# Optimization experiments

Measured on AMD Instinct MI355X. Metric: run time of the kernel, lower is better.

Reference implementation:

```python
import jax, jax.numpy as jnp
import numpy as np

N = 8192
IN_F = 64
OUT_F = 64
ALPHA = 0.2
NEG_INF = -9e15
DENSITY = 0.02


def _signed_sparse(key, shape, density):
    k1, k2 = jax.random.split(key)
    mask = jax.random.uniform(k1, shape) < density
    vals = jax.random.normal(k2, shape, dtype=jnp.float32)
    return jnp.where(mask, vals, 0.0)


def setup_inputs() -> dict:
    key = jax.random.key(0)
    k_h, k_na, k_ea, k_w, k_a = jax.random.split(key, 5)
    h = jax.random.normal(k_h, (N, IN_F), dtype=jnp.float32)
    node_adj = _signed_sparse(k_na, (N, N), DENSITY)
    edge_adj = _signed_sparse(k_ea, (N, N), DENSITY)
    # xavier_uniform with gain=1.414
    lim_w = 1.414 * np.sqrt(6.0 / (IN_F + OUT_F))
    W_att = jax.random.uniform(k_w, (IN_F, OUT_F), minval=-lim_w, maxval=lim_w, dtype=jnp.float32)
    lim_a = 1.414 * np.sqrt(6.0 / (OUT_F + 1))
    a = jax.random.uniform(k_a, (OUT_F, 1), minval=-lim_a, maxval=lim_a, dtype=jnp.float32)
    return {"h": h, "node_adj": node_adj, "edge_adj": edge_adj, "W_att": W_att, "a": a}


def reference(h, node_adj, edge_adj, W_att, a):
    # h: [N, F_in], node_adj/edge_adj: [N, N]
    h_att = h @ W_att                                   # [N, F_out]
    h_plus = (node_adj > 0).astype(h.dtype) @ h_att     # [N, F_out]
    h_minus = (node_adj < 0).astype(h.dtype) @ h_att    # [N, F_out]
    a_input = jnp.abs(h_plus - h_minus)                 # [N, F_out]
    e = jax.nn.leaky_relu(a_input @ a, ALPHA)           # [N, 1]
    e_row = e[:, 0][None, :]                            # broadcast: row i of scores = e^T
    scores = jnp.where(edge_adj != 0, e_row, jnp.float32(NEG_INF))  # [N, N]
    attention = jax.nn.softmax(scores, axis=1)          # [N, N]
    # dropout omitted (eval-mode reference)
    h_prime = (attention * edge_adj) @ h                # [N, F_in]
    return h_prime, attention
```

## Files before the change

kernel.cpp:

```cpp
#include <hip/hip_runtime.h>
#include <math.h>

#define NN 8192
#define FF 64
#define ALPHA 0.2f
#define ECAP 512
#define WCAP 256

typedef float vf4 __attribute__((ext_vector_type(4)));

__global__ __launch_bounds__(256) void k_hatt(const float* __restrict__ h,
                                              const float* __restrict__ W,
                                              float* __restrict__ h_att) {
    __shared__ float Ws[64 * 64];
    int t = threadIdx.x;
    for (int k = t; k < 64 * 64; k += 256) Ws[k] = W[k];
    __syncthreads();
    int idx = blockIdx.x * 256 + t;
    int r = idx >> 6, c = idx & 63;
    const float* hr = h + (size_t)r * FF;
    float acc = 0.f;
#pragma unroll
    for (int k = 0; k < 64; ++k) acc += hr[k] * Ws[k * 64 + c];
    h_att[idx] = acc;
}

__global__ __launch_bounds__(256) void k_e(const float* __restrict__ node_adj,
                                           const float* __restrict__ h_att,
                                           const float* __restrict__ a,
                                           float* __restrict__ e) {
    __shared__ int lists[4][ECAP];
    int t = threadIdx.x, w = t >> 6, lane = t & 63;
    int row = blockIdx.x * 4 + w;
    unsigned long long lmask = (1ull << lane) - 1ull;
    const vf4* rp = (const vf4*)(node_adj + (size_t)row * NN);
    int cnt = 0;
#pragma unroll 4
    for (int it = 0; it < 32; ++it) {
        int idx = it * 64 + lane;
        vf4 v = __builtin_nontemporal_load(rp + idx);
        int j0 = idx * 4;
        { bool nz = v.x != 0.f; unsigned long long m = __ballot(nz);
          if (nz) lists[w][cnt + __popcll(m & lmask)] = (v.x > 0.f) ? (j0 + 1) : -(j0 + 1);
          cnt += __popcll(m); }
        { bool nz = v.y != 0.f; unsigned long long m = __ballot(nz);
          if (nz) lists[w][cnt + __popcll(m & lmask)] = (v.y > 0.f) ? (j0 + 2) : -(j0 + 2);
          cnt += __popcll(m); }
        { bool nz = v.z != 0.f; unsigned long long m = __ballot(nz);
          if (nz) lists[w][cnt + __popcll(m & lmask)] = (v.z > 0.f) ? (j0 + 3) : -(j0 + 3);
          cnt += __popcll(m); }
        { bool nz = v.w != 0.f; unsigned long long m = __ballot(nz);
          if (nz) lists[w][cnt + __popcll(m & lmask)] = (v.w > 0.f) ? (j0 + 4) : -(j0 + 4);
          cnt += __popcll(m); }
    }
    __syncthreads();

    float acc = 0.f;
    for (int k = 0; k < cnt; ++k) {
        int code = lists[w][k];
        int j = (code < 0 ? -code : code) - 1;
        float hv = h_att[(size_t)j * FF + lane];
        acc += (code < 0) ? -hv : hv;
    }
    float v = fabsf(acc) * a[lane];
#pragma unroll
    for (int off = 32; off; off >>= 1) v += __shfl_down(v, off, 64);
    if (lane == 0) e[row] = (v > 0.f) ? v : ALPHA * v;
}

__global__ __launch_bounds__(256) void k_prep(const float* __restrict__ e,
                                              float* __restrict__ E) {
    __shared__ float red[256];
    int t = threadIdx.x;
    float lm = -3.0e38f;
    for (int k = t; k < NN; k += 256) lm = fmaxf(lm, e[k]);
    red[t] = lm; __syncthreads();
    for (int s = 128; s; s >>= 1) { if (t < s) red[t] = fmaxf(red[t], red[t + s]); __syncthreads(); }
    float m = red[0];
    int i = blockIdx.x * 256 + t;
    E[i] = __expf(e[i] - m);
}

__global__ __launch_bounds__(256) void k_att(const float* __restrict__ edge_adj,
                                             const float* __restrict__ E,
                                             const float* __restrict__ h,
                                             float* __restrict__ att_out,
                                             float* __restrict__ hprime) {
    __shared__ int   jseg[4][WCAP];
    __shared__ float vseg[4][WCAP];
    __shared__ float red[256];
    __shared__ float r4z[4];
    __shared__ int   cnts[4];
    int t = threadIdx.x, w = t >> 6, lane = t & 63;
    int row = blockIdx.x;
    unsigned long long lmask = (1ull << lane) - 1ull;

    const vf4* rp = (const vf4*)(edge_adj + (size_t)row * NN);
    const vf4* Ep = (const vf4*)E;
    vf4 o[8];
    float zloc = 0.f;
    int cnt = 0;
#pragma unroll
    for (int it = 0; it < 8; ++it) {
        int idx = it * 256 + t;
        vf4 v  = __builtin_nontemporal_load(rp + idx);
        vf4 Ev = Ep[idx];
        int j0 = idx * 4;
        { bool nz = v.x != 0.f; unsigned long long m = __ballot(nz);
          float ox = nz ? Ev.x : 0.f;
          if (nz) { int p = cnt + __popcll(m & lmask); jseg[w][p] = j0;     vseg[w][p] = v.x * Ev.x; }
          cnt += __popcll(m); zloc += ox; o[it].x = ox; }
        { bool nz = v.y != 0.f; unsigned long long m = __ballot(nz);
          float oy = nz ? Ev.y : 0.f;
          if (nz) { int p = cnt + __popcll(m & lmask); jseg[w][p] = j0 + 1; vseg[w][p] = v.y * Ev.y; }
          cnt += __popcll(m); zloc += oy; o[it].y = oy; }
        { bool nz = v.z != 0.f; unsigned long long m = __ballot(nz);
          float oz = nz ? Ev.z : 0.f;
          if (nz) { int p = cnt + __popcll(m & lmask); jseg[w][p] = j0 + 2; vseg[w][p] = v.z * Ev.z; }
          cnt += __popcll(m); zloc += oz; o[it].z = oz; }
        { bool nz = v.w != 0.f; unsigned long long m = __ballot(nz);
          float ow = nz ? Ev.w : 0.f;
          if (nz) { int p = cnt + __popcll(m & lmask); jseg[w][p] = j0 + 3; vseg[w][p] = v.w * Ev.w; }
          cnt += __popcll(m); zloc += ow; o[it].w = ow; }
    }
    if (lane == 0) cnts[w] = cnt;
#pragma unroll
    for (int off = 32; off; off >>= 1) zloc += __shfl_down(zloc, off, 64);
    if (lane == 0) r4z[w] = zloc;
    __syncthreads();
    float Z = r4z[0] + r4z[1] + r4z[2] + r4z[3];
    int tot = cnts[0] + cnts[1] + cnts[2] + cnts[3];
    float invZ = (tot > 0) ? 1.f / Z : 0.f;

    float acc = 0.f;
    for (int k = 0; k < cnt; ++k)
        acc += vseg[w][k] * h[(size_t)jseg[w][k] * FF + lane];
    red[t] = acc;
    __syncthreads();
    if (t < 64)
        hprime[(size_t)row * FF + t] = (red[t] + red[t + 64] + red[t + 128] + red[t + 192]) * invZ;

    vf4* ap = (vf4*)(att_out + (size_t)row * NN);
    float unif = 1.0f / NN;
#pragma unroll
    for (int it = 0; it < 8; ++it) {
        int idx = it * 256 + t;
        vf4 ov = o[it];
        ov.x *= invZ; ov.y *= invZ; ov.z *= invZ; ov.w *= invZ;
        if (tot == 0) { ov.x = unif; ov.y = unif; ov.z = unif; ov.w = unif; }
        __builtin_nontemporal_store(ov, ap + idx);
    }
}

extern "C" void kernel_launch(void* const* d_in, const int* in_sizes, int n_in,
                              void* d_out, int out_size, void* d_ws, size_t ws_size,
                              hipStream_t stream) {
    const float* h        = (const float*)d_in[0];
    const float* node_adj = (const float*)d_in[1];
    const float* edge_adj = (const float*)d_in[2];
    const float* W_att    = (const float*)d_in[3];
    const float* a        = (const float*)d_in[4];

    float* out    = (float*)d_out;
    float* hprime = out;
    float* att    = out + (size_t)NN * FF;

    float* h_att = (float*)d_ws;
    float* e_vec = h_att + (size_t)NN * FF;
    float* E_vec = e_vec + NN;

    k_hatt<<<(NN * FF) / 256, 256, 0, stream>>>(h, W_att, h_att);
    k_e<<<NN / 4, 256, 0, stream>>>(node_adj, h_att, a, e_vec);
    k_prep<<<NN / 256, 256, 0, stream>>>(e_vec, E_vec);
    k_att<<<NN, 256, 0, stream>>>(edge_adj, E_vec, h, att, hprime);
}
```

Before: 627.5 us.

## Process four sparse neighbors per wave with float4 gathers and mbcnt prefix

The sparse gather loops in the score and attention kernels are restructured so each wave handles four list entries per iteration: 16 lanes per entry each load a float4 of the 64-wide feature row. Partial sums are then combined with xor shuffles. Lane prefix counts now use the mbcnt intrinsics, and index/value pairs are packed into a single int2 shared entry. The lists are padded with zero entries so the loop can run in steps of four. This cuts serial loop iterations and widens memory accesses, in exchange for extra shuffle reductions and padding reads of row 0.

```diff
diff --git a/kernel.cpp b/kernel.cpp
--- a/kernel.cpp
+++ b/kernel.cpp
@@ -8,6 +8,11 @@
 #define WCAP 256
 
 typedef float vf4 __attribute__((ext_vector_type(4)));
+
+__device__ __forceinline__ unsigned mbcnt64(unsigned long long m) {
+    return __builtin_amdgcn_mbcnt_hi((unsigned)(m >> 32),
+           __builtin_amdgcn_mbcnt_lo((unsigned)m, 0u));
+}
 
 __global__ __launch_bounds__(256) void k_hatt(const float* __restrict__ h,
                                               const float* __restrict__ W,
@@ -32,7 +37,6 @@
     __shared__ int lists[4][ECAP];
     int t = threadIdx.x, w = t >> 6, lane = t & 63;
     int row = blockIdx.x * 4 + w;
-    unsigned long long lmask = (1ull << lane) - 1ull;
     const vf4* rp = (const vf4*)(node_adj + (size_t)row * NN);
     int cnt = 0;
 #pragma unroll 4
@@ -41,30 +45,45 @@
         vf4 v = __builtin_nontemporal_load(rp + idx);
         int j0 = idx * 4;
         { bool nz = v.x != 0.f; unsigned long long m = __ballot(nz);
-          if (nz) lists[w][cnt + __popcll(m & lmask)] = (v.x > 0.f) ? (j0 + 1) : -(j0 + 1);
+          if (nz) lists[w][cnt + mbcnt64(m)] = (v.x > 0.f) ? (j0 + 1) : -(j0 + 1);
           cnt += __popcll(m); }
         { bool nz = v.y != 0.f; unsigned long long m = __ballot(nz);
-          if (nz) lists[w][cnt + __popcll(m & lmask)] = (v.y > 0.f) ? (j0 + 2) : -(j0 + 2);
+          if (nz) lists[w][cnt + mbcnt64(m)] = (v.y > 0.f) ? (j0 + 2) : -(j0 + 2);
           cnt += __popcll(m); }
         { bool nz = v.z != 0.f; unsigned long long m = __ballot(nz);
-          if (nz) lists[w][cnt + __popcll(m & lmask)] = (v.z > 0.f) ? (j0 + 3) : -(j0 + 3);
+          if (nz) lists[w][cnt + mbcnt64(m)] = (v.z > 0.f) ? (j0 + 3) : -(j0 + 3);
           cnt += __popcll(m); }
         { bool nz = v.w != 0.f; unsigned long long m = __ballot(nz);
-          if (nz) lists[w][cnt + __popcll(m & lmask)] = (v.w > 0.f) ? (j0 + 4) : -(j0 + 4);
-          cnt += __popcll(m); }
-    }
-    __syncthreads();
-
-    float acc = 0.f;
-    for (int k = 0; k < cnt; ++k) {
-        int code = lists[w][k];
-        int j = (code < 0 ? -code : code) - 1;
-        float hv = h_att[(size_t)j * FF + lane];
-        acc += (code < 0) ? -hv : hv;
-    }
-    float v = fabsf(acc) * a[lane];
-#pragma unroll
-    for (int off = 32; off; off >>= 1) v += __shfl_down(v, off, 64);
+          if (nz) lists[w][cnt + mbcnt64(m)] = (v.w > 0.f) ? (j0 + 4) : -(j0 + 4);
+          cnt += __popcll(m); }
+    }
+    if (lane < 4) lists[w][cnt + lane] = 0;
+
+    int g = lane >> 4, fl = lane & 15;
+    const vf4* Hp = (const vf4*)h_att;
+    vf4 acc = {0.f, 0.f, 0.f, 0.f};
+    int cnt4 = (cnt + 3) & ~3;
+#pragma unroll 2
+    for (int k = 0; k < cnt4; k += 4) {
+        int code = lists[w][k + g];
+        float s = (code < 0) ? -1.f : (code > 0 ? 1.f : 0.f);
+        int aj = (code < 0) ? -code : code;
+        int j = (aj > 0) ? aj - 1 : 0;
+        vf4 hv = Hp[(size_t)j * 16 + fl];
+        acc.x += s * hv.x; acc.y += s * hv.y; acc.z += s * hv.z; acc.w += s * hv.w;
+    }
+    acc.x += __shfl_xor(acc.x, 16, 64); acc.y += __shfl_xor(acc.y, 16, 64);
+    acc.z += __shfl_xor(acc.z, 16, 64); acc.w += __shfl_xor(acc.w, 16, 64);
+    acc.x += __shfl_xor(acc.x, 32, 64); acc.y += __shfl_xor(acc.y, 32, 64);
+    acc.z += __shfl_xor(acc.z, 32, 64); acc.w += __shfl_xor(acc.w, 32, 64);
+
+    vf4 av = ((const vf4*)a)[fl];
+    float v = fabsf(acc.x) * av.x + fabsf(acc.y) * av.y +
+              fabsf(acc.z) * av.z + fabsf(acc.w) * av.w;
+    v += __shfl_down(v, 8, 64);
+    v += __shfl_down(v, 4, 64);
+    v += __shfl_down(v, 2, 64);
+    v += __shfl_down(v, 1, 64);
     if (lane == 0) e[row] = (v > 0.f) ? v : ALPHA * v;
 }
 
@@ -86,14 +105,12 @@
                                              const float* __restrict__ h,
                                              float* __restrict__ att_out,
                                              float* __restrict__ hprime) {
-    __shared__ int   jseg[4][WCAP];
-    __shared__ float vseg[4][WCAP];
-    __shared__ float red[256];
+    __shared__ int2 seg[4][WCAP];
+    __shared__ vf4  red4[64];
     __shared__ float r4z[4];
     __shared__ int   cnts[4];
     int t = threadIdx.x, w = t >> 6, lane = t & 63;
     int row = blockIdx.x;
-    unsigned long long lmask = (1ull << lane) - 1ull;
 
     const vf4* rp = (const vf4*)(edge_adj + (size_t)row * NN);
     const vf4* Ep = (const vf4*)E;
@@ -108,35 +125,49 @@
         int j0 = idx * 4;
         { bool nz = v.x != 0.f; unsigned long long m = __ballot(nz);
           float ox = nz ? Ev.x : 0.f;
-          if (nz) { int p = cnt + __popcll(m & lmask); jseg[w][p] = j0;     vseg[w][p] = v.x * Ev.x; }
+          if (nz) seg[w][cnt + mbcnt64(m)] = make_int2(j0,     __float_as_int(v.x * Ev.x));
           cnt += __popcll(m); zloc += ox; o[it].x = ox; }
         { bool nz = v.y != 0.f; unsigned long long m = __ballot(nz);
           float oy = nz ? Ev.y : 0.f;
-          if (nz) { int p = cnt + __popcll(m & lmask); jseg[w][p] = j0 + 1; vseg[w][p] = v.y * Ev.y; }
+          if (nz) seg[w][cnt + mbcnt64(m)] = make_int2(j0 + 1, __float_as_int(v.y * Ev.y));
           cnt += __popcll(m); zloc += oy; o[it].y = oy; }
         { bool nz = v.z != 0.f; unsigned long long m = __ballot(nz);
           float oz = nz ? Ev.z : 0.f;
-          if (nz) { int p = cnt + __popcll(m & lmask); jseg[w][p] = j0 + 2; vseg[w][p] = v.z * Ev.z; }
+          if (nz) seg[w][cnt + mbcnt64(m)] = make_int2(j0 + 2, __float_as_int(v.z * Ev.z));
           cnt += __popcll(m); zloc += oz; o[it].z = oz; }
         { bool nz = v.w != 0.f; unsigned long long m = __ballot(nz);
           float ow = nz ? Ev.w : 0.f;
-          if (nz) { int p = cnt + __popcll(m & lmask); jseg[w][p] = j0 + 3; vseg[w][p] = v.w * Ev.w; }
+          if (nz) seg[w][cnt + mbcnt64(m)] = make_int2(j0 + 3, __float_as_int(v.w * Ev.w));
           cnt += __popcll(m); zloc += ow; o[it].w = ow; }
     }
     if (lane == 0) cnts[w] = cnt;
 #pragma unroll
     for (int off = 32; off; off >>= 1) zloc += __shfl_down(zloc, off, 64);
     if (lane == 0) r4z[w] = zloc;
+    if (lane < 4) seg[w][cnt + lane] = make_int2(0, 0);
     __syncthreads();
     float Z = r4z[0] + r4z[1] + r4z[2] + r4z[3];
     int tot = cnts[0] + cnts[1] + cnts[2] + cnts[3];
     float invZ = (tot > 0) ? 1.f / Z : 0.f;
 
-    float acc = 0.f;
-    for (int k = 0; k < cnt; ++k)
-        acc += vseg[w][k] * h[(size_t)jseg[w][k] * FF + lane];
-    red[t] = acc;
+    int g = lane >> 4, fl = lane & 15;
+    const vf4* Hp = (const vf4*)h;
+    vf4 acc = {0.f, 0.f, 0.f, 0.f};
+    int cnt4 = (cnt + 3) & ~3;
+#pragma unroll 2
+    for (int k = 0; k < cnt4; k += 4) {
+        int2 sv = seg[w][k + g];
+        float vv = __int_as_float(sv.y);
+        vf4 hv = Hp[(size_t)sv.x * 16 + fl];
+        acc.x += vv * hv.x; acc.y += vv * hv.y; acc.z += vv * hv.z; acc.w += vv * hv.w;
+    }
+    acc.x += __shfl_xor(acc.x, 16, 64); acc.y += __shfl_xor(acc.y, 16, 64);
+    acc.z += __shfl_xor(acc.z, 16, 64); acc.w += __shfl_xor(acc.w, 16, 64);
+    acc.x += __shfl_xor(acc.x, 32, 64); acc.y += __shfl_xor(acc.y, 32, 64);
+    acc.z += __shfl_xor(acc.z, 32, 64); acc.w += __shfl_xor(acc.w, 32, 64);
+    if (lane < 16) red4[w * 16 + fl] = acc;
     __syncthreads();
+    const float* red = (const float*)red4;
     if (t < 64)
         hprime[(size_t)row * FF + t] = (red[t] + red[t + 64] + red[t + 128] + red[t + 192]) * invZ;
 
```

Measured after the change: 616.6 us. About the same (-1.7%).
